# Optimization experiments

Hardware: AMD Instinct MI355X
Metric: run time of the kernel (lower is better)

The kernel has to match this reference:

```python
import jax, jax.numpy as jnp
import numpy as np

DIM = 64
N_NODES = 20000
N_EDGES = 60000
N_TORS = 1024
ACT = 6


def setup_inputs() -> dict:
    key = jax.random.key(0)
    ks = iter(jax.random.split(key, 40))
    def rn(*s):
        return jax.random.normal(next(ks), s, dtype=jnp.float32) * 0.05
    d = DIM
    inp = {}
    inp["x"] = jax.random.normal(next(ks), (N_NODES, 3), dtype=jnp.float32)
    inp["edge_attr"] = jax.random.uniform(next(ks), (N_EDGES, 7), dtype=jnp.float32)
    inp["W0"] = rn(d, 3); inp["b0"] = rn(d)
    inp["We1"] = rn(128, 7); inp["be1"] = rn(128)
    inp["We2"] = rn(d * d, 128); inp["be2"] = rn(d * d)
    inp["root"] = rn(d, d); inp["conv_b"] = rn(d)
    inp["gru_wih"] = rn(3 * d, d); inp["gru_whh"] = rn(3 * d, d)
    inp["gru_bih"] = rn(3 * d); inp["gru_bhh"] = rn(3 * d)
    inp["s2s_wi"] = rn(4 * d, 2 * d); inp["s2s_wh"] = rn(4 * d, d)
    inp["s2s_bi"] = rn(4 * d); inp["s2s_bh"] = rn(4 * d)
    inp["mem_wi"] = rn(24 * d, 6 * d); inp["mem_wh"] = rn(24 * d, 6 * d)
    inp["mem_bi"] = rn(24 * d); inp["mem_bh"] = rn(24 * d)
    inp["W1"] = rn(2 * d, 6 * d); inp["b1"] = rn(2 * d)
    inp["W2"] = rn(ACT, 2 * d); inp["b2"] = rn(ACT)
    inp["edge_index"] = jax.random.randint(next(ks), (2, N_EDGES), 0, N_NODES)
    inp["nonring"] = jax.random.randint(next(ks), (N_TORS, 4), 0, N_NODES)
    return inp


def reference(x, edge_attr, W0, b0, We1, be1, We2, be2, root, conv_b,
              gru_wih, gru_whh, gru_bih, gru_bhh,
              s2s_wi, s2s_wh, s2s_bi, s2s_bh,
              mem_wi, mem_wh, mem_bi, mem_bh,
              W1, b1, W2, b2, edge_index, nonring):
    d = DIM
    n = x.shape[0]
    src, dst = edge_index[0], edge_index[1]
    # lin0 + relu
    out = jax.nn.relu(x @ W0.T + b0)                       # [N, d]
    h = out                                                # GRU hidden
    # per-edge dim x dim weights from the edge MLP (edge_attr is loop-invariant)
    We = jax.nn.relu(edge_attr @ We1.T + be1) @ We2.T + be2
    We = We.reshape(-1, d, d)                              # [E, d, d]
    deg = jnp.zeros((n,), jnp.float32).at[dst].add(1.0)
    inv_deg = 1.0 / jnp.maximum(deg, 1.0)
    for _ in range(6):
        # NNConv: gather -> per-edge matmul -> scatter-mean, plus root transform
        msg = jnp.einsum('ed,edf->ef', out[src], We)       # [E, d]
        agg = jnp.zeros((n, d), msg.dtype).at[dst].add(msg) * inv_deg[:, None]
        m = jax.nn.relu(agg + out @ root + conv_b)
        # GRU cell (torch gate order r, z, n)
        gx = m @ gru_wih.T + gru_bih
        gh = h @ gru_whh.T + gru_bhh
        r = jax.nn.sigmoid(gx[:, :d] + gh[:, :d])
        z = jax.nn.sigmoid(gx[:, d:2 * d] + gh[:, d:2 * d])
        nn_ = jnp.tanh(gx[:, 2 * d:] + r * gh[:, 2 * d:])
        h = (1.0 - z) * nn_ + z * h
        out = h
    # Set2Set pooling, single graph (data.batch is all zeros)
    q_star = jnp.zeros((1, 2 * d), out.dtype)
    hs = jnp.zeros((1, d), out.dtype)
    cs = jnp.zeros((1, d), out.dtype)
    for _ in range(6):
        g = q_star @ s2s_wi.T + s2s_bi + hs @ s2s_wh.T + s2s_bh
        i = jax.nn.sigmoid(g[:, :d])
        f = jax.nn.sigmoid(g[:, d:2 * d])
        gg = jnp.tanh(g[:, 2 * d:3 * d])
        o = jax.nn.sigmoid(g[:, 3 * d:])
        cs = f * cs + i * gg
        hs = o * jnp.tanh(cs)
        q = hs                                             # [1, d]
        e = out @ q[0]                                     # [N]
        a = jax.nn.softmax(e)
        rvec = (a[:, None] * out).sum(0, keepdims=True)    # [1, d]
        q_star = jnp.concatenate([q, rvec], axis=1)
    pool = q_star                                          # [1, 2d]
    # faithful quirky index/view/permute + repeat_interleave concat
    t = nonring.shape[0]
    sel = out[nonring.reshape(-1)]                         # [4T, d]
    sel = sel.reshape(4 * d, t).T                          # [T, 4d]
    rep = jnp.repeat(pool.reshape(-1), t).reshape(t, 2 * d)
    z_in = jnp.concatenate([sel, rep], axis=1)             # [T, 6d]
    # memory LSTM, seq_len = 1, zero initial state (states not passed in orig)
    D6 = 6 * d
    g = z_in @ mem_wi.T + mem_bi + mem_bh                  # h0 = 0 so Wh term vanishes
    i = jax.nn.sigmoid(g[:, :D6])
    f = jax.nn.sigmoid(g[:, D6:2 * D6])
    gg = jnp.tanh(g[:, 2 * D6:3 * D6])
    o = jax.nn.sigmoid(g[:, 3 * D6:])
    cm = i * gg
    hm = o * jnp.tanh(cm)                                  # [T, 6d]
    y = jax.nn.relu(hm @ W1.T + b1) @ W2.T + b2            # [T, ACT]
    return y[None]                                         # [1, T, ACT]
```

## Files before the change

kernel.cpp:

```cpp
#include <hip/hip_runtime.h>
#include <hip/hip_bf16.h>

#define NN 20000
#define NE 60000
#define NT 1024

typedef unsigned short ushortT;
typedef __attribute__((ext_vector_type(8))) short bf16x8;
typedef __attribute__((ext_vector_type(8))) unsigned short u16x8;
typedef __attribute__((ext_vector_type(4))) float f32x4;

__device__ __forceinline__ float sigm(float x){ return 1.0f/(1.0f+expf(-x)); }
__device__ __forceinline__ float bfu2f(ushortT u){ return __uint_as_float(((unsigned)u)<<16); }
__device__ __forceinline__ ushortT f2bfu(float f){
  __hip_bfloat16 b = __float2bfloat16(f);
  return *reinterpret_cast<ushortT*>(&b);
}

__global__ void k_lin0(const float* __restrict__ x, const float* __restrict__ W0,
                       const float* __restrict__ b0, float* __restrict__ out,
                       float* __restrict__ h, ushortT* __restrict__ outbf){
  int idx = blockIdx.x*256 + threadIdx.x;
  int n = idx >> 6, j = idx & 63;
  float a = b0[j] + x[n*3+0]*W0[j*3+0] + x[n*3+1]*W0[j*3+1] + x[n*3+2]*W0[j*3+2];
  a = fmaxf(a, 0.0f);
  out[idx] = a; h[idx] = a; outbf[idx] = f2bfu(a);
}

__global__ void k_deg(const int* __restrict__ dst, float* __restrict__ deg){
  int e = blockIdx.x*256 + threadIdx.x;
  if (e < NE) atomicAdd(&deg[dst[e]], 1.0f);
}

__global__ void k_edgemlp(const float* __restrict__ ea, const float* __restrict__ We1,
                          const float* __restrict__ be1, ushortT* __restrict__ Rbf){
  int idx = blockIdx.x*256 + threadIdx.x;
  int e = idx >> 7, k = idx & 127;
  float a = be1[k];
  #pragma unroll
  for (int j = 0; j < 7; ++j) a += ea[e*7+j]*We1[k*7+j];
  Rbf[idx] = f2bfu(fmaxf(a, 0.0f));
}

#define PREP_T ((4096*128) + (1536*384) + (128*384) + 2*(192*64))
__global__ void k_prep(const float* __restrict__ We2, const float* __restrict__ memwi,
                       const float* __restrict__ W1, const float* __restrict__ gwih,
                       const float* __restrict__ gwhh,
                       ushortT* __restrict__ We2bf, ushortT* __restrict__ wmem,
                       ushortT* __restrict__ w1bf, float* __restrict__ gwih_t,
                       float* __restrict__ gwhh_t){
  int idx = blockIdx.x*256 + threadIdx.x;
  if (idx < 4096*128){ We2bf[idx] = f2bfu(We2[idx]); return; }
  idx -= 4096*128;
  if (idx < 1536*384){ wmem[idx] = f2bfu(memwi[idx]); return; }
  idx -= 1536*384;
  if (idx < 128*384){ w1bf[idx] = f2bfu(W1[idx]); return; }
  idx -= 128*384;
  if (idx < 192*64){ int r = idx / 64, c = idx % 64; gwih_t[c*192 + r] = gwih[idx]; return; }
  idx -= 192*64;
  if (idx < 192*64){ int r = idx / 64, c = idx % 64; gwhh_t[c*192 + r] = gwhh[idx]; return; }
}

#define EB 256
__global__ __launch_bounds__(256, 2) void k_fmsg(
    const ushortT* __restrict__ Rbf, const ushortT* __restrict__ We2bf,
    const float* __restrict__ be2, const ushortT* __restrict__ outbf,
    const int* __restrict__ src, const int* __restrict__ dst,
    float* __restrict__ agg)
{
  __shared__ ushortT o_sT[64][264];
  __shared__ ushortT bufB[4][4096];
  __shared__ float   be2q[64][32];
  __shared__ int     dst_s[EB];

  int tid = threadIdx.x;
  int e0 = blockIdx.x * EB;
  int fh = blockIdx.y;
  int w = tid >> 6, lane = tid & 63;
  int l15 = lane & 15, g = lane >> 4;

  auto stage = [&](int d, int b){
    #pragma unroll
    for (int i = 0; i < 2; ++i){
      int s = (w*2 + i)*64 + lane;
      int row = s >> 4, kslot = s & 15;
      const ushortT* gp = We2bf + (size_t)((d<<6) + (fh<<5) + row)*128 + ((kslot ^ (row & 7))<<3);
      __builtin_amdgcn_global_load_lds(
          (const __attribute__((address_space(1))) void*)gp,
          (__attribute__((address_space(3))) void*)&bufB[b][(size_t)s*8], 16, 0, 0);
    }
  };
  stage(0, 0); stage(1, 1); stage(2, 2);

  {
    int ge = e0 + tid;
    int sn = src[ge];
    dst_s[tid] = (ge < NE) ? dst[ge] : -1;
    const ushortT* op = outbf + (size_t)sn*64;
    #pragma unroll
    for (int i = 0; i < 8; ++i){
      u16x8 v = *reinterpret_cast<const u16x8*>(op + i*8);
      #pragma unroll
      for (int j = 0; j < 8; ++j) o_sT[i*8+j][tid] = v[j];
    }
  }
  #pragma unroll
  for (int i = 0; i < 8; ++i){
    int idx = tid*8 + i;
    int dd = idx >> 5, cc = idx & 31;
    be2q[dd][cc] = be2[(dd<<6) + (fh<<5) + cc];
  }

  bf16x8 af[4][4];
  #pragma unroll
  for (int t = 0; t < 4; ++t){
    #pragma unroll
    for (int ks = 0; ks < 4; ++ks){
      int ge = e0 + w*64 + t*16 + l15;
      bf16x8 z = {0,0,0,0,0,0,0,0};
      af[t][ks] = (ge < NE) ? *reinterpret_cast<const bf16x8*>(Rbf + (size_t)ge*128 + ks*32 + g*8) : z;
    }
  }

  f32x4 msg[4][2];
  #pragma unroll
  for (int t = 0; t < 4; ++t){
    #pragma unroll
    for (int q = 0; q < 2; ++q){ msg[t][q][0]=0.f; msg[t][q][1]=0.f; msg[t][q][2]=0.f; msg[t][q][3]=0.f; }
  }
  __syncthreads();

  auto compute = [&](int d, int b){
    bf16x8 bf0[4], bf1[4];
    #pragma unroll
    for (int ks = 0; ks < 4; ++ks){
      bf0[ks] = *reinterpret_cast<const bf16x8*>(&bufB[b][ (l15)*128    + ((((ks<<2)+g) ^ (l15&7))<<3) ]);
      bf1[ks] = *reinterpret_cast<const bf16x8*>(&bufB[b][ (16+l15)*128 + ((((ks<<2)+g) ^ (l15&7))<<3) ]);
    }
    f32x4 ac[4][2];
    #pragma unroll
    for (int t = 0; t < 4; ++t){
      #pragma unroll
      for (int q = 0; q < 2; ++q){ ac[t][q][0]=0.f; ac[t][q][1]=0.f; ac[t][q][2]=0.f; ac[t][q][3]=0.f; }
    }
    __builtin_amdgcn_s_setprio(1);
    #pragma unroll
    for (int ks = 0; ks < 4; ++ks){
      #pragma unroll
      for (int t = 0; t < 4; ++t){
        ac[t][0] = __builtin_amdgcn_mfma_f32_16x16x32_bf16(af[t][ks], bf0[ks], ac[t][0], 0, 0, 0);
        ac[t][1] = __builtin_amdgcn_mfma_f32_16x16x32_bf16(af[t][ks], bf1[ks], ac[t][1], 0, 0, 0);
      }
    }
    __builtin_amdgcn_s_setprio(0);
    float be2v0 = be2q[d][l15];
    float be2v1 = be2q[d][16 + l15];
    #pragma unroll
    for (int t = 0; t < 4; ++t){
      ushort4 ou = *reinterpret_cast<const ushort4*>(&o_sT[d][w*64 + t*16 + g*4]);
      float o0 = bfu2f(ou.x), o1 = bfu2f(ou.y), o2 = bfu2f(ou.z), o3 = bfu2f(ou.w);
      msg[t][0][0] += o0*(ac[t][0][0] + be2v0);
      msg[t][0][1] += o1*(ac[t][0][1] + be2v0);
      msg[t][0][2] += o2*(ac[t][0][2] + be2v0);
      msg[t][0][3] += o3*(ac[t][0][3] + be2v0);
      msg[t][1][0] += o0*(ac[t][1][0] + be2v1);
      msg[t][1][1] += o1*(ac[t][1][1] + be2v1);
      msg[t][1][2] += o2*(ac[t][1][2] + be2v1);
      msg[t][1][3] += o3*(ac[t][1][3] + be2v1);
    }
  };

  for (int d = 0; d < 61; ++d){
    asm volatile("s_waitcnt vmcnt(4)" ::: "memory");
    __builtin_amdgcn_sched_barrier(0);
    __builtin_amdgcn_s_barrier();
    __builtin_amdgcn_sched_barrier(0);
    stage(d + 3, (d + 3) & 3);
    compute(d, d & 3);
  }
  asm volatile("s_waitcnt vmcnt(4)" ::: "memory");
  __builtin_amdgcn_sched_barrier(0);
  __builtin_amdgcn_s_barrier();
  __builtin_amdgcn_sched_barrier(0);
  compute(61, 61 & 3);
  asm volatile("s_waitcnt vmcnt(2)" ::: "memory");
  __builtin_amdgcn_sched_barrier(0);
  __builtin_amdgcn_s_barrier();
  __builtin_amdgcn_sched_barrier(0);
  compute(62, 62 & 3);
  asm volatile("s_waitcnt vmcnt(0)" ::: "memory");
  __builtin_amdgcn_sched_barrier(0);
  __builtin_amdgcn_s_barrier();
  __builtin_amdgcn_sched_barrier(0);
  compute(63, 63 & 3);

  #pragma unroll
  for (int t = 0; t < 4; ++t){
    #pragma unroll
    for (int r = 0; r < 4; ++r){
      int el = w*64 + t*16 + g*4 + r;
      int tn = dst_s[el];
      if (tn >= 0){
        atomicAdd(&agg[(size_t)tn*64 + (fh<<5) + l15],      msg[t][0][r]);
        atomicAdd(&agg[(size_t)tn*64 + (fh<<5) + 16 + l15], msg[t][1][r]);
      }
    }
  }
}

__global__ void k_gru(const float* __restrict__ agg_in, const float* __restrict__ deg,
                      const float* __restrict__ root, const float* __restrict__ conv_b,
                      const float* __restrict__ wih_t, const float* __restrict__ whh_t,
                      const float* __restrict__ bih, const float* __restrict__ bhh,
                      float* __restrict__ out, float* __restrict__ h,
                      ushortT* __restrict__ outbf){
  __shared__ float os[16][64], hsm[16][64], ms[16][64];
  float* agg = const_cast<float*>(agg_in);
  int tid = threadIdx.x;
  int j = tid & 63, sub = tid >> 6;
  int n0 = blockIdx.x * 16;
  #pragma unroll
  for (int i = 0; i < 4; ++i){
    int nl = sub + 4*i;
    os[nl][j]  = out[(size_t)(n0+nl)*64 + j];
    hsm[nl][j] = h[(size_t)(n0+nl)*64 + j];
  }
  __syncthreads();
  float a[4];
  #pragma unroll
  for (int i = 0; i < 4; ++i){
    int nl = sub + 4*i;
    float inv = 1.0f/fmaxf(deg[n0+nl], 1.0f);
    a[i] = agg[(size_t)(n0+nl)*64 + j]*inv + conv_b[j];
    agg[(size_t)(n0+nl)*64 + j] = 0.0f;
  }
  for (int d = 0; d < 64; ++d){
    float rdj = root[d*64 + j];
    #pragma unroll
    for (int i = 0; i < 4; ++i) a[i] += os[sub + 4*i][d]*rdj;
  }
  #pragma unroll
  for (int i = 0; i < 4; ++i) ms[sub + 4*i][j] = fmaxf(a[i], 0.0f);
  __syncthreads();
  float gxr[4], gxz[4], gxn[4], ghr[4], ghz[4], ghn[4];
  #pragma unroll
  for (int i = 0; i < 4; ++i){
    gxr[i] = bih[j];     gxz[i] = bih[64+j];  gxn[i] = bih[128+j];
    ghr[i] = bhh[j];     ghz[i] = bhh[64+j];  ghn[i] = bhh[128+j];
  }
  for (int d = 0; d < 64; ++d){
    float wir = wih_t[d*192 + j], wiz = wih_t[d*192 + 64 + j], win = wih_t[d*192 + 128 + j];
    float whr = whh_t[d*192 + j], whz = whh_t[d*192 + 64 + j], whn = whh_t[d*192 + 128 + j];
    #pragma unroll
    for (int i = 0; i < 4; ++i){
      float mv = ms[sub + 4*i][d], hv = hsm[sub + 4*i][d];
      gxr[i] += mv*wir; gxz[i] += mv*wiz; gxn[i] += mv*win;
      ghr[i] += hv*whr; ghz[i] += hv*whz; ghn[i] += hv*whn;
    }
  }
  #pragma unroll
  for (int i = 0; i < 4; ++i){
    int nl = sub + 4*i;
    float r = sigm(gxr[i]+ghr[i]), zg = sigm(gxz[i]+ghz[i]);
    float nn_ = tanhf(gxn[i] + r*ghn[i]);
    float hn = (1.0f - zg)*nn_ + zg*hsm[nl][j];
    h[(size_t)(n0+nl)*64 + j]   = hn;
    out[(size_t)(n0+nl)*64 + j] = hn;
    outbf[(size_t)(n0+nl)*64 + j] = f2bfu(hn);
  }
}

__global__ void k_s2s2(const float* __restrict__ out, const float* __restrict__ wi,
                       const float* __restrict__ wh, const float* __restrict__ bi,
                       const float* __restrict__ bh, float* __restrict__ st, int it){
  const float* sr = st + it*256;
  float* sw = st + (it+1)*256;
  __shared__ float qs[128], hsl[64], gg[256];
  __shared__ float ob[128*65], wl[128], zred[128], part[256];
  int tid = threadIdx.x;
  int n0 = blockIdx.x * 128;

  if (tid < 64) qs[tid] = sr[tid];
  else if (tid < 128){
    float Z = sr[192];
    qs[tid] = (Z != 0.0f) ? sr[128 + (tid-64)]/Z : 0.0f;
  }
  __syncthreads();
  {
    float a = bi[tid] + bh[tid];
    #pragma unroll 8
    for (int k = 0; k < 128; ++k) a += qs[k]*wi[tid*128 + k];
    #pragma unroll 8
    for (int k = 0; k < 64;  ++k) a += sr[k]*wh[tid*64 + k];
    gg[tid] = a;
  }
  __syncthreads();
  if (tid < 64){
    float iv = sigm(gg[tid]), fv = sigm(gg[64+tid]);
    float gv = tanhf(gg[128+tid]), ov = sigm(gg[192+tid]);
    float c = fv*sr[64+tid] + iv*gv;
    float hnew = ov*tanhf(c);
    hsl[tid] = hnew;
    if (blockIdx.x == 0){ sw[64+tid] = c; sw[tid] = hnew; }
  }
  #pragma unroll
  for (int rr = 0; rr < 8; ++rr){
    int idx = rr*1024 + tid*4;
    int nl = idx >> 6, jj = idx & 63;
    float4 v = make_float4(0.f,0.f,0.f,0.f);
    if (n0 + nl < NN) v = *reinterpret_cast<const float4*>(&out[(size_t)(n0+nl)*64 + jj]);
    ob[nl*65 + jj + 0] = v.x; ob[nl*65 + jj + 1] = v.y;
    ob[nl*65 + jj + 2] = v.z; ob[nl*65 + jj + 3] = v.w;
  }
  __syncthreads();
  if (tid < 128){
    float e = 0.f;
    #pragma unroll 8
    for (int jj = 0; jj < 64; ++jj) e += ob[tid*65 + jj]*hsl[jj];
    float wv = (n0 + tid < NN) ? expf(e) : 0.f;
    wl[tid] = wv; zred[tid] = wv;
  }
  __syncthreads();
  if (tid < 64) zred[tid] += zred[tid + 64];
  __syncthreads();
  if (tid < 32) zred[tid] += zred[tid + 32];
  __syncthreads();
  if (tid < 16) zred[tid] += zred[tid + 16];
  __syncthreads();
  if (tid < 8) zred[tid] += zred[tid + 8];
  __syncthreads();
  if (tid == 0){
    float z = zred[0]+zred[1]+zred[2]+zred[3]+zred[4]+zred[5]+zred[6]+zred[7];
    atomicAdd(&sw[192], z);
  }
  {
    int gq = tid >> 6, d = tid & 63;
    float acc = 0.f;
    #pragma unroll 8
    for (int i = 0; i < 32; ++i){
      int nl = gq*32 + i;
      acc += wl[nl]*ob[nl*65 + d];
    }
    part[tid] = acc;
  }
  __syncthreads();
  if (tid < 64)
    atomicAdd(&sw[128 + tid], part[tid] + part[64+tid] + part[128+tid] + part[192+tid]);
}

__global__ void k_z(const float* __restrict__ out, const float* __restrict__ st,
                    const int* __restrict__ nonring, ushortT* __restrict__ zbf){
  const float* s6 = st + 6*256;
  int idx = blockIdx.x*256 + threadIdx.x;
  int t = idx / 384, c = idx % 384;
  float v;
  if (c < 256){
    int a = c*16 + (t >> 6);
    int node = nonring[a];
    v = out[(size_t)node*64 + (t & 63)];
  } else {
    int pi = t >> 3;
    v = (pi < 64) ? s6[pi] : s6[128 + (pi - 64)] / s6[192];
  }
  zbf[idx] = f2bfu(v);
}

__global__ __launch_bounds__(256) void k_mem2(
    const ushortT* __restrict__ zbf, const ushortT* __restrict__ wmem,
    const float* __restrict__ membi, const float* __restrict__ membh,
    ushortT* __restrict__ hmbf){
  int tid = threadIdx.x;
  int w = tid >> 6, lane = tid & 63;
  int l15 = lane & 15, g = lane >> 4;
  int m0 = blockIdx.x * 32;
  int jw = blockIdx.y * 64 + w * 16;

  f32x4 ai[2], ag[2], ao[2];
  #pragma unroll
  for (int m = 0; m < 2; ++m){
    #pragma unroll
    for (int r = 0; r < 4; ++r){ ai[m][r]=0.f; ag[m][r]=0.f; ao[m][r]=0.f; }
  }
  const ushortT* a0p = zbf + (size_t)(m0 + l15)*384 + g*8;
  const ushortT* a1p = zbf + (size_t)(m0 + 16 + l15)*384 + g*8;
  const ushortT* bip = wmem + (size_t)(jw + l15)*384 + g*8;
  const ushortT* bgp = wmem + (size_t)(768 + jw + l15)*384 + g*8;
  const ushortT* bop = wmem + (size_t)(1152 + jw + l15)*384 + g*8;
  #pragma unroll
  for (int ks = 0; ks < 12; ++ks){
    bf16x8 a0 = *reinterpret_cast<const bf16x8*>(a0p + ks*32);
    bf16x8 a1 = *reinterpret_cast<const bf16x8*>(a1p + ks*32);
    bf16x8 bi = *reinterpret_cast<const bf16x8*>(bip + ks*32);
    bf16x8 bg = *reinterpret_cast<const bf16x8*>(bgp + ks*32);
    bf16x8 bo = *reinterpret_cast<const bf16x8*>(bop + ks*32);
    ai[0] = __builtin_amdgcn_mfma_f32_16x16x32_bf16(a0, bi, ai[0], 0, 0, 0);
    ai[1] = __builtin_amdgcn_mfma_f32_16x16x32_bf16(a1, bi, ai[1], 0, 0, 0);
    ag[0] = __builtin_amdgcn_mfma_f32_16x16x32_bf16(a0, bg, ag[0], 0, 0, 0);
    ag[1] = __builtin_amdgcn_mfma_f32_16x16x32_bf16(a1, bg, ag[1], 0, 0, 0);
    ao[0] = __builtin_amdgcn_mfma_f32_16x16x32_bf16(a0, bo, ao[0], 0, 0, 0);
    ao[1] = __builtin_amdgcn_mfma_f32_16x16x32_bf16(a1, bo, ao[1], 0, 0, 0);
  }
  int j = jw + l15;
  float bI = membi[j]        + membh[j];
  float bG = membi[768 + j]  + membh[768 + j];
  float bO = membi[1152 + j] + membh[1152 + j];
  #pragma unroll
  for (int m = 0; m < 2; ++m){
    #pragma unroll
    for (int r = 0; r < 4; ++r){
      int t = m0 + m*16 + g*4 + r;
      float gi = ai[m][r] + bI;
      float gG = ag[m][r] + bG;
      float go = ao[m][r] + bO;
      float cm = sigm(gi)*tanhf(gG);
      hmbf[(size_t)t*384 + j] = f2bfu(sigm(go)*tanhf(cm));
    }
  }
}

__global__ __launch_bounds__(256) void k_fin1(
    const ushortT* __restrict__ hmbf, const ushortT* __restrict__ w1bf,
    const float* __restrict__ b1, float* __restrict__ hid){
  int tid = threadIdx.x;
  int w = tid >> 6, lane = tid & 63;
  int l15 = lane & 15, g = lane >> 4;
  int m0 = blockIdx.x * 32;
  int cw = blockIdx.y * 64 + w * 16;

  f32x4 acc[2];
  #pragma unroll
  for (int m = 0; m < 2; ++m){
    #pragma unroll
    for (int r = 0; r < 4; ++r) acc[m][r] = 0.f;
  }
  const ushortT* a0p = hmbf + (size_t)(m0 + l15)*384 + g*8;
  const ushortT* a1p = hmbf + (size_t)(m0 + 16 + l15)*384 + g*8;
  const ushortT* bp  = w1bf + (size_t)(cw + l15)*384 + g*8;
  #pragma unroll
  for (int ks = 0; ks < 12; ++ks){
    bf16x8 a0 = *reinterpret_cast<const bf16x8*>(a0p + ks*32);
    bf16x8 a1 = *reinterpret_cast<const bf16x8*>(a1p + ks*32);
    bf16x8 b  = *reinterpret_cast<const bf16x8*>(bp + ks*32);
    acc[0] = __builtin_amdgcn_mfma_f32_16x16x32_bf16(a0, b, acc[0], 0, 0, 0);
    acc[1] = __builtin_amdgcn_mfma_f32_16x16x32_bf16(a1, b, acc[1], 0, 0, 0);
  }
  int c = cw + l15;
  float bv = b1[c];
  #pragma unroll
  for (int m = 0; m < 2; ++m){
    #pragma unroll
    for (int r = 0; r < 4; ++r){
      int t = m0 + m*16 + g*4 + r;
      hid[(size_t)t*128 + c] = fmaxf(acc[m][r] + bv, 0.0f);
    }
  }
}

__global__ void k_fin2(const float* __restrict__ hid, const float* __restrict__ W2,
                       const float* __restrict__ b2, float* __restrict__ y){
  int tid = threadIdx.x;
  int t = blockIdx.x*32 + (tid >> 3);
  int j = tid & 7;
  if (j >= 6) return;
  float a = b2[j];
  const float* hp = hid + (size_t)t*128;
  const float* wp = W2 + j*128;
  #pragma unroll 8
  for (int k = 0; k < 128; ++k) a += hp[k]*wp[k];
  y[t*6 + j] = a;
}

extern "C" void kernel_launch(void* const* d_in, const int* in_sizes, int n_in,
                              void* d_out, int out_size, void* d_ws, size_t ws_size,
                              hipStream_t stream){
  const float* x      = (const float*)d_in[0];
  const float* ea     = (const float*)d_in[1];
  const float* W0     = (const float*)d_in[2];
  const float* b0     = (const float*)d_in[3];
  const float* We1    = (const float*)d_in[4];
  const float* be1    = (const float*)d_in[5];
  const float* We2    = (const float*)d_in[6];
  const float* be2    = (const float*)d_in[7];
  const float* root   = (const float*)d_in[8];
  const float* conv_b = (const float*)d_in[9];
  const float* gwih   = (const float*)d_in[10];
  const float* gwhh   = (const float*)d_in[11];
  const float* gbih   = (const float*)d_in[12];
  const float* gbhh   = (const float*)d_in[13];
  const float* s2swi  = (const float*)d_in[14];
  const float* s2swh  = (const float*)d_in[15];
  const float* s2sbi  = (const float*)d_in[16];
  const float* s2sbh  = (const float*)d_in[17];
  const float* memwi  = (const float*)d_in[18];
  const float* membi  = (const float*)d_in[20];
  const float* membh  = (const float*)d_in[21];
  const float* W1     = (const float*)d_in[22];
  const float* b1     = (const float*)d_in[23];
  const float* W2     = (const float*)d_in[24];
  const float* b2     = (const float*)d_in[25];
  const int*   eidx   = (const int*)d_in[26];
  const int*   nonr   = (const int*)d_in[27];
  const int* src = eidx, *dst = eidx + NE;
  float* y = (float*)d_out;

  char* wsb = (char*)d_ws;
  size_t off = 0;
  auto alloc = [&](size_t bytes){ size_t o = off; off += (bytes + 255) & ~(size_t)255; return o; };
  float* out    = (float*)(wsb + alloc((size_t)NN*64*4));
  float* h      = (float*)(wsb + alloc((size_t)NN*64*4));
  float* agg    = (float*)(wsb + alloc((size_t)NN*64*4));
  float* deg    = (float*)(wsb + alloc((size_t)NN*4));
  float* st     = (float*)(wsb + alloc(7*256*4));
  float* hid    = (float*)(wsb + alloc((size_t)NT*128*4));
  float* gwih_t = (float*)(wsb + alloc((size_t)192*64*4));
  float* gwhh_t = (float*)(wsb + alloc((size_t)192*64*4));
  ushortT* Rbf  = (ushortT*)(wsb + alloc((size_t)NE*128*2));
  ushortT* We2bf= (ushortT*)(wsb + alloc((size_t)4096*128*2));
  ushortT* wmem = (ushortT*)(wsb + alloc((size_t)1536*384*2));
  ushortT* w1bf = (ushortT*)(wsb + alloc((size_t)128*384*2));
  ushortT* zbf  = (ushortT*)(wsb + alloc((size_t)NT*384*2));
  ushortT* hmbf = (ushortT*)(wsb + alloc((size_t)NT*384*2));
  ushortT* outbf= (ushortT*)(wsb + alloc((size_t)NN*64*2));
  (void)ws_size; (void)n_in; (void)in_sizes; (void)out_size;

  hipMemsetAsync(deg, 0, (size_t)NN*4, stream);
  hipMemsetAsync(st, 0, 7*256*4, stream);
  hipMemsetAsync(agg, 0, (size_t)NN*64*4, stream);
  k_lin0<<<NN*64/256, 256, 0, stream>>>(x, W0, b0, out, h, outbf);
  k_deg<<<(NE+255)/256, 256, 0, stream>>>(dst, deg);
  k_edgemlp<<<NE*128/256, 256, 0, stream>>>(ea, We1, be1, Rbf);
  k_prep<<<(PREP_T+255)/256, 256, 0, stream>>>(We2, memwi, W1, gwih, gwhh,
                                               We2bf, wmem, w1bf, gwih_t, gwhh_t);

  for (int it = 0; it < 6; ++it){
    k_fmsg<<<dim3((NE + EB - 1)/EB, 2), 256, 0, stream>>>(Rbf, We2bf, be2, outbf, src, dst, agg);
    k_gru<<<NN/16, 256, 0, stream>>>(agg, deg, root, conv_b, gwih_t, gwhh_t,
                                     gbih, gbhh, out, h, outbf);
  }

  for (int it = 0; it < 6; ++it){
    k_s2s2<<<(NN + 127)/128, 256, 0, stream>>>(out, s2swi, s2swh, s2sbi, s2sbh, st, it);
  }

  k_z<<<NT*384/256, 256, 0, stream>>>(out, st, nonr, zbf);
  k_mem2<<<dim3(32, 6), 256, 0, stream>>>(zbf, wmem, membi, membh, hmbf);
  k_fin1<<<dim3(32, 2), 256, 0, stream>>>(hmbf, w1bf, b1, hid);
  k_fin2<<<32, 256, 0, stream>>>(hid, W2, b2, y);
}
```

Baseline: 764.3 us.

## Software-pipeline LDS fragment reads one stage ahead of MFMA compute

Splits the per-slice compute into a fragment-read phase and an MFMA phase. The B fragments and o values for slice d+1 are read from LDS while the MFMAs for slice d run, so LDS latency is hidden behind matrix work. To keep slice d+1 ready one iteration early, the global-load wait is tightened from vmcnt(4) to vmcnt(2). This doubles the fragment registers held per thread, which may lower occupancy, and it shortens the prefetch distance for global loads.

After: 783.6 us. 1.03x slower.

```diff
diff --git a/kernel.cpp b/kernel.cpp
--- a/kernel.cpp
+++ b/kernel.cpp
@@ -130,13 +130,21 @@
   }
   __syncthreads();
 
-  auto compute = [&](int d, int b){
-    bf16x8 bf0[4], bf1[4];
+  bf16x8 bcur0[4], bcur1[4], bnxt0[4], bnxt1[4];
+  ushort4 ocur[4], onxt[4];
+
+  auto readfrags = [&](int d, int b, bf16x8* f0, bf16x8* f1, ushort4* ov){
     #pragma unroll
     for (int ks = 0; ks < 4; ++ks){
-      bf0[ks] = *reinterpret_cast<const bf16x8*>(&bufB[b][ (l15)*128    + ((((ks<<2)+g) ^ (l15&7))<<3) ]);
-      bf1[ks] = *reinterpret_cast<const bf16x8*>(&bufB[b][ (16+l15)*128 + ((((ks<<2)+g) ^ (l15&7))<<3) ]);
-    }
+      f0[ks] = *reinterpret_cast<const bf16x8*>(&bufB[b][ (l15)*128    + ((((ks<<2)+g) ^ (l15&7))<<3) ]);
+      f1[ks] = *reinterpret_cast<const bf16x8*>(&bufB[b][ (16+l15)*128 + ((((ks<<2)+g) ^ (l15&7))<<3) ]);
+    }
+    #pragma unroll
+    for (int t = 0; t < 4; ++t)
+      ov[t] = *reinterpret_cast<const ushort4*>(&o_sT[d][w*64 + t*16 + g*4]);
+  };
+
+  auto domfma = [&](int d, const bf16x8* f0, const bf16x8* f1, const ushort4* ov){
     f32x4 ac[4][2];
     #pragma unroll
     for (int t = 0; t < 4; ++t){
@@ -148,8 +156,8 @@
     for (int ks = 0; ks < 4; ++ks){
       #pragma unroll
       for (int t = 0; t < 4; ++t){
-        ac[t][0] = __builtin_amdgcn_mfma_f32_16x16x32_bf16(af[t][ks], bf0[ks], ac[t][0], 0, 0, 0);
-        ac[t][1] = __builtin_amdgcn_mfma_f32_16x16x32_bf16(af[t][ks], bf1[ks], ac[t][1], 0, 0, 0);
+        ac[t][0] = __builtin_amdgcn_mfma_f32_16x16x32_bf16(af[t][ks], f0[ks], ac[t][0], 0, 0, 0);
+        ac[t][1] = __builtin_amdgcn_mfma_f32_16x16x32_bf16(af[t][ks], f1[ks], ac[t][1], 0, 0, 0);
       }
     }
     __builtin_amdgcn_s_setprio(0);
@@ -157,8 +165,7 @@
     float be2v1 = be2q[d][16 + l15];
     #pragma unroll
     for (int t = 0; t < 4; ++t){
-      ushort4 ou = *reinterpret_cast<const ushort4*>(&o_sT[d][w*64 + t*16 + g*4]);
-      float o0 = bfu2f(ou.x), o1 = bfu2f(ou.y), o2 = bfu2f(ou.z), o3 = bfu2f(ou.w);
+      float o0 = bfu2f(ov[t].x), o1 = bfu2f(ov[t].y), o2 = bfu2f(ov[t].z), o3 = bfu2f(ov[t].w);
       msg[t][0][0] += o0*(ac[t][0][0] + be2v0);
       msg[t][0][1] += o1*(ac[t][0][1] + be2v0);
       msg[t][0][2] += o2*(ac[t][0][2] + be2v0);
@@ -170,29 +177,38 @@
     }
   };
 
+  readfrags(0, 0, bcur0, bcur1, ocur);
+
   for (int d = 0; d < 61; ++d){
-    asm volatile("s_waitcnt vmcnt(4)" ::: "memory");
+    asm volatile("s_waitcnt vmcnt(2)" ::: "memory");
     __builtin_amdgcn_sched_barrier(0);
     __builtin_amdgcn_s_barrier();
     __builtin_amdgcn_sched_barrier(0);
     stage(d + 3, (d + 3) & 3);
-    compute(d, d & 3);
-  }
-  asm volatile("s_waitcnt vmcnt(4)" ::: "memory");
-  __builtin_amdgcn_sched_barrier(0);
-  __builtin_amdgcn_s_barrier();
-  __builtin_amdgcn_sched_barrier(0);
-  compute(61, 61 & 3);
+    readfrags(d + 1, (d + 1) & 3, bnxt0, bnxt1, onxt);
+    domfma(d, bcur0, bcur1, ocur);
+    #pragma unroll
+    for (int ks = 0; ks < 4; ++ks){ bcur0[ks] = bnxt0[ks]; bcur1[ks] = bnxt1[ks]; }
+    #pragma unroll
+    for (int t = 0; t < 4; ++t) ocur[t] = onxt[t];
+  }
   asm volatile("s_waitcnt vmcnt(2)" ::: "memory");
   __builtin_amdgcn_sched_barrier(0);
   __builtin_amdgcn_s_barrier();
   __builtin_amdgcn_sched_barrier(0);
-  compute(62, 62 & 3);
+  readfrags(62, 62 & 3, bnxt0, bnxt1, onxt);
+  domfma(61, bcur0, bcur1, ocur);
+  #pragma unroll
+  for (int ks = 0; ks < 4; ++ks){ bcur0[ks] = bnxt0[ks]; bcur1[ks] = bnxt1[ks]; }
+  #pragma unroll
+  for (int t = 0; t < 4; ++t) ocur[t] = onxt[t];
   asm volatile("s_waitcnt vmcnt(0)" ::: "memory");
   __builtin_amdgcn_sched_barrier(0);
   __builtin_amdgcn_s_barrier();
   __builtin_amdgcn_sched_barrier(0);
-  compute(63, 63 & 3);
+  readfrags(63, 63 & 3, bnxt0, bnxt1, onxt);
+  domfma(62, bcur0, bcur1, ocur);
+  domfma(63, bnxt0, bnxt1, onxt);
 
   #pragma unroll
   for (int t = 0; t < 4; ++t){
```

## Rewrite GRU node update with bf16 MFMA for root and gate matmuls

Applied to the files above, without the earlier changes.

Replaces the scalar fp32 GRU/root-transform kernel with an MFMA-based version that computes the root transform and the input/hidden gate matmuls as bf16 16x16x32 tiles over 32 nodes per block. Weights are pre-converted to bf16 (root transposed) in the prep kernel, and a bf16 copy of the hidden state is kept. The intent is to remove the heavy per-thread FMA loops and LDS reads of the old kernel. The cost is bf16 rounding of the hidden state and messages inside the recurrence, which may reduce accuracy.

Measured after the change: 680.1 us. 11.0% less time.

```diff
diff --git a/kernel.cpp b/kernel.cpp
--- a/kernel.cpp
+++ b/kernel.cpp
@@ -19,12 +19,15 @@
 
 __global__ void k_lin0(const float* __restrict__ x, const float* __restrict__ W0,
                        const float* __restrict__ b0, float* __restrict__ out,
-                       float* __restrict__ h, ushortT* __restrict__ outbf){
+                       float* __restrict__ h, ushortT* __restrict__ outbf,
+                       ushortT* __restrict__ hbf){
   int idx = blockIdx.x*256 + threadIdx.x;
   int n = idx >> 6, j = idx & 63;
   float a = b0[j] + x[n*3+0]*W0[j*3+0] + x[n*3+1]*W0[j*3+1] + x[n*3+2]*W0[j*3+2];
   a = fmaxf(a, 0.0f);
-  out[idx] = a; h[idx] = a; outbf[idx] = f2bfu(a);
+  out[idx] = a; h[idx] = a;
+  ushortT u = f2bfu(a);
+  outbf[idx] = u; hbf[idx] = u;
 }
 
 __global__ void k_deg(const int* __restrict__ dst, float* __restrict__ deg){
@@ -42,13 +45,13 @@
   Rbf[idx] = f2bfu(fmaxf(a, 0.0f));
 }
 
-#define PREP_T ((4096*128) + (1536*384) + (128*384) + 2*(192*64))
+#define PREP_T ((4096*128) + (1536*384) + (128*384) + (192*64) + (192*64) + (64*64))
 __global__ void k_prep(const float* __restrict__ We2, const float* __restrict__ memwi,
                        const float* __restrict__ W1, const float* __restrict__ gwih,
-                       const float* __restrict__ gwhh,
+                       const float* __restrict__ gwhh, const float* __restrict__ root,
                        ushortT* __restrict__ We2bf, ushortT* __restrict__ wmem,
-                       ushortT* __restrict__ w1bf, float* __restrict__ gwih_t,
-                       float* __restrict__ gwhh_t){
+                       ushortT* __restrict__ w1bf, ushortT* __restrict__ gwihbf,
+                       ushortT* __restrict__ gwhhbf, ushortT* __restrict__ rootTbf){
   int idx = blockIdx.x*256 + threadIdx.x;
   if (idx < 4096*128){ We2bf[idx] = f2bfu(We2[idx]); return; }
   idx -= 4096*128;
@@ -56,9 +59,11 @@
   idx -= 1536*384;
   if (idx < 128*384){ w1bf[idx] = f2bfu(W1[idx]); return; }
   idx -= 128*384;
-  if (idx < 192*64){ int r = idx / 64, c = idx % 64; gwih_t[c*192 + r] = gwih[idx]; return; }
+  if (idx < 192*64){ gwihbf[idx] = f2bfu(gwih[idx]); return; }
   idx -= 192*64;
-  if (idx < 192*64){ int r = idx / 64, c = idx % 64; gwhh_t[c*192 + r] = gwhh[idx]; return; }
+  if (idx < 192*64){ gwhhbf[idx] = f2bfu(gwhh[idx]); return; }
+  idx -= 192*64;
+  if (idx < 64*64){ int d = idx >> 6, j = idx & 63; rootTbf[j*64 + d] = f2bfu(root[idx]); }
 }
 
 #define EB 256
@@ -208,65 +213,103 @@
   }
 }
 
-__global__ void k_gru(const float* __restrict__ agg_in, const float* __restrict__ deg,
-                      const float* __restrict__ root, const float* __restrict__ conv_b,
-                      const float* __restrict__ wih_t, const float* __restrict__ whh_t,
-                      const float* __restrict__ bih, const float* __restrict__ bhh,
-                      float* __restrict__ out, float* __restrict__ h,
-                      ushortT* __restrict__ outbf){
-  __shared__ float os[16][64], hsm[16][64], ms[16][64];
+__global__ __launch_bounds__(256) void k_gru2(
+    const float* __restrict__ agg_in, const float* __restrict__ deg,
+    const ushortT* __restrict__ rootT, const float* __restrict__ conv_b,
+    const ushortT* __restrict__ wih, const ushortT* __restrict__ whh,
+    const float* __restrict__ bih, const float* __restrict__ bhh,
+    float* __restrict__ out, float* __restrict__ h,
+    ushortT* __restrict__ outbf, ushortT* __restrict__ hbf)
+{
+  __shared__ ushortT mbf[32*64];
   float* agg = const_cast<float*>(agg_in);
   int tid = threadIdx.x;
-  int j = tid & 63, sub = tid >> 6;
-  int n0 = blockIdx.x * 16;
-  #pragma unroll
-  for (int i = 0; i < 4; ++i){
-    int nl = sub + 4*i;
-    os[nl][j]  = out[(size_t)(n0+nl)*64 + j];
-    hsm[nl][j] = h[(size_t)(n0+nl)*64 + j];
-  }
-  __syncthreads();
-  float a[4];
-  #pragma unroll
-  for (int i = 0; i < 4; ++i){
-    int nl = sub + 4*i;
-    float inv = 1.0f/fmaxf(deg[n0+nl], 1.0f);
-    a[i] = agg[(size_t)(n0+nl)*64 + j]*inv + conv_b[j];
-    agg[(size_t)(n0+nl)*64 + j] = 0.0f;
-  }
-  for (int d = 0; d < 64; ++d){
-    float rdj = root[d*64 + j];
-    #pragma unroll
-    for (int i = 0; i < 4; ++i) a[i] += os[sub + 4*i][d]*rdj;
-  }
-  #pragma unroll
-  for (int i = 0; i < 4; ++i) ms[sub + 4*i][j] = fmaxf(a[i], 0.0f);
-  __syncthreads();
-  float gxr[4], gxz[4], gxn[4], ghr[4], ghz[4], ghn[4];
-  #pragma unroll
-  for (int i = 0; i < 4; ++i){
-    gxr[i] = bih[j];     gxz[i] = bih[64+j];  gxn[i] = bih[128+j];
-    ghr[i] = bhh[j];     ghz[i] = bhh[64+j];  ghn[i] = bhh[128+j];
-  }
-  for (int d = 0; d < 64; ++d){
-    float wir = wih_t[d*192 + j], wiz = wih_t[d*192 + 64 + j], win = wih_t[d*192 + 128 + j];
-    float whr = whh_t[d*192 + j], whz = whh_t[d*192 + 64 + j], whn = whh_t[d*192 + 128 + j];
-    #pragma unroll
-    for (int i = 0; i < 4; ++i){
-      float mv = ms[sub + 4*i][d], hv = hsm[sub + 4*i][d];
-      gxr[i] += mv*wir; gxz[i] += mv*wiz; gxn[i] += mv*win;
-      ghr[i] += hv*whr; ghz[i] += hv*whz; ghn[i] += hv*whn;
-    }
-  }
-  #pragma unroll
-  for (int i = 0; i < 4; ++i){
-    int nl = sub + 4*i;
-    float r = sigm(gxr[i]+ghr[i]), zg = sigm(gxz[i]+ghz[i]);
-    float nn_ = tanhf(gxn[i] + r*ghn[i]);
-    float hn = (1.0f - zg)*nn_ + zg*hsm[nl][j];
-    h[(size_t)(n0+nl)*64 + j]   = hn;
-    out[(size_t)(n0+nl)*64 + j] = hn;
-    outbf[(size_t)(n0+nl)*64 + j] = f2bfu(hn);
+  int w = tid >> 6, lane = tid & 63;
+  int l15 = lane & 15, g = lane >> 4;
+  int n0 = blockIdx.x * 32;
+  int j = w*16 + l15;
+
+  f32x4 acc1[2];
+  #pragma unroll
+  for (int rt = 0; rt < 2; ++rt){ acc1[rt][0]=0.f; acc1[rt][1]=0.f; acc1[rt][2]=0.f; acc1[rt][3]=0.f; }
+  bf16x8 ah[2][2];
+  #pragma unroll
+  for (int ks = 0; ks < 2; ++ks){
+    bf16x8 b = *reinterpret_cast<const bf16x8*>(rootT + (size_t)j*64 + g*8 + ks*32);
+    #pragma unroll
+    for (int rt = 0; rt < 2; ++rt){
+      bf16x8 a = *reinterpret_cast<const bf16x8*>(outbf + (size_t)(n0 + rt*16 + l15)*64 + g*8 + ks*32);
+      acc1[rt] = __builtin_amdgcn_mfma_f32_16x16x32_bf16(a, b, acc1[rt], 0, 0, 0);
+      ah[rt][ks] = *reinterpret_cast<const bf16x8*>(hbf + (size_t)(n0 + rt*16 + l15)*64 + g*8 + ks*32);
+    }
+  }
+  {
+    float cb = conv_b[j];
+    #pragma unroll
+    for (int rt = 0; rt < 2; ++rt){
+      #pragma unroll
+      for (int r = 0; r < 4; ++r){
+        int row = rt*16 + g*4 + r;
+        int node = n0 + row;
+        float inv = 1.0f/fmaxf(deg[node], 1.0f);
+        float mval = fmaxf(acc1[rt][r] + agg[(size_t)node*64 + j]*inv + cb, 0.0f);
+        agg[(size_t)node*64 + j] = 0.0f;
+        int gran = (j >> 3) ^ (row & 7);
+        mbf[row*64 + (gran<<3) + (j & 7)] = f2bfu(mval);
+      }
+    }
+  }
+  __syncthreads();
+
+  f32x4 gx[3][2], gh[3][2];
+  #pragma unroll
+  for (int ci = 0; ci < 3; ++ci){
+    #pragma unroll
+    for (int rt = 0; rt < 2; ++rt){
+      gx[ci][rt][0]=0.f; gx[ci][rt][1]=0.f; gx[ci][rt][2]=0.f; gx[ci][rt][3]=0.f;
+      gh[ci][rt][0]=0.f; gh[ci][rt][1]=0.f; gh[ci][rt][2]=0.f; gh[ci][rt][3]=0.f;
+    }
+  }
+  #pragma unroll
+  for (int ks = 0; ks < 2; ++ks){
+    bf16x8 am[2];
+    #pragma unroll
+    for (int rt = 0; rt < 2; ++rt){
+      int arow = rt*16 + l15;
+      int agran = (g + ks*4) ^ (l15 & 7);
+      am[rt] = *reinterpret_cast<const bf16x8*>(&mbf[arow*64 + (agran<<3)]);
+    }
+    #pragma unroll
+    for (int ci = 0; ci < 3; ++ci){
+      int c = (w + ci*4)*16 + l15;
+      bf16x8 bx = *reinterpret_cast<const bf16x8*>(wih + (size_t)c*64 + g*8 + ks*32);
+      bf16x8 bh = *reinterpret_cast<const bf16x8*>(whh + (size_t)c*64 + g*8 + ks*32);
+      #pragma unroll
+      for (int rt = 0; rt < 2; ++rt){
+        gx[ci][rt] = __builtin_amdgcn_mfma_f32_16x16x32_bf16(am[rt], bx, gx[ci][rt], 0, 0, 0);
+        gh[ci][rt] = __builtin_amdgcn_mfma_f32_16x16x32_bf16(ah[rt][ks], bh, gh[ci][rt], 0, 0, 0);
+      }
+    }
+  }
+  float bxr = bih[j], bxz = bih[64+j], bxn = bih[128+j];
+  float bhr = bhh[j], bhz = bhh[64+j], bhn = bhh[128+j];
+  #pragma unroll
+  for (int rt = 0; rt < 2; ++rt){
+    #pragma unroll
+    for (int r = 0; r < 4; ++r){
+      int node = n0 + rt*16 + g*4 + r;
+      float gxr = gx[0][rt][r] + bxr, gxz = gx[1][rt][r] + bxz, gxn = gx[2][rt][r] + bxn;
+      float ghr = gh[0][rt][r] + bhr, ghz = gh[1][rt][r] + bhz, ghn = gh[2][rt][r] + bhn;
+      float rr = sigm(gxr + ghr), zz = sigm(gxz + ghz);
+      float nn_ = tanhf(gxn + rr*ghn);
+      float hold = h[(size_t)node*64 + j];
+      float hn = (1.0f - zz)*nn_ + zz*hold;
+      h[(size_t)node*64 + j]   = hn;
+      out[(size_t)node*64 + j] = hn;
+      ushortT u = f2bfu(hn);
+      outbf[(size_t)node*64 + j] = u;
+      hbf[(size_t)node*64 + j]   = u;
+    }
   }
 }
 
@@ -512,8 +555,6 @@
   float* deg    = (float*)(wsb + alloc((size_t)NN*4));
   float* st     = (float*)(wsb + alloc(7*256*4));
   float* hid    = (float*)(wsb + alloc((size_t)NT*128*4));
-  float* gwih_t = (float*)(wsb + alloc((size_t)192*64*4));
-  float* gwhh_t = (float*)(wsb + alloc((size_t)192*64*4));
   ushortT* Rbf  = (ushortT*)(wsb + alloc((size_t)NE*128*2));
   ushortT* We2bf= (ushortT*)(wsb + alloc((size_t)4096*128*2));
   ushortT* wmem = (ushortT*)(wsb + alloc((size_t)1536*384*2));
@@ -521,21 +562,25 @@
   ushortT* zbf  = (ushortT*)(wsb + alloc((size_t)NT*384*2));
   ushortT* hmbf = (ushortT*)(wsb + alloc((size_t)NT*384*2));
   ushortT* outbf= (ushortT*)(wsb + alloc((size_t)NN*64*2));
+  ushortT* hbf  = (ushortT*)(wsb + alloc((size_t)NN*64*2));
+  ushortT* gwihbf = (ushortT*)(wsb + alloc((size_t)192*64*2));
+  ushortT* gwhhbf = (ushortT*)(wsb + alloc((size_t)192*64*2));
+  ushortT* rootTbf= (ushortT*)(wsb + alloc((size_t)64*64*2));
   (void)ws_size; (void)n_in; (void)in_sizes; (void)out_size;
 
   hipMemsetAsync(deg, 0, (size_t)NN*4, stream);
   hipMemsetAsync(st, 0, 7*256*4, stream);
   hipMemsetAsync(agg, 0, (size_t)NN*64*4, stream);
-  k_lin0<<<NN*64/256, 256, 0, stream>>>(x, W0, b0, out, h, outbf);
+  k_lin0<<<NN*64/256, 256, 0, stream>>>(x, W0, b0, out, h, outbf, hbf);
   k_deg<<<(NE+255)/256, 256, 0, stream>>>(dst, deg);
   k_edgemlp<<<NE*128/256, 256, 0, stream>>>(ea, We1, be1, Rbf);
-  k_prep<<<(PREP_T+255)/256, 256, 0, stream>>>(We2, memwi, W1, gwih, gwhh,
-                                               We2bf, wmem, w1bf, gwih_t, gwhh_t);
+  k_prep<<<(PREP_T+255)/256, 256, 0, stream>>>(We2, memwi, W1, gwih, gwhh, root,
+                                               We2bf, wmem, w1bf, gwihbf, gwhhbf, rootTbf);
 
   for (int it = 0; it < 6; ++it){
     k_fmsg<<<dim3((NE + EB - 1)/EB, 2), 256, 0, stream>>>(Rbf, We2bf, be2, outbf, src, dst, agg);
-    k_gru<<<NN/16, 256, 0, stream>>>(agg, deg, root, conv_b, gwih_t, gwhh_t,
-                                     gbih, gbhh, out, h, outbf);
+    k_gru2<<<NN/32, 256, 0, stream>>>(agg, deg, rootTbf, conv_b, gwihbf, gwhhbf,
+                                      gbih, gbhh, out, h, outbf, hbf);
   }
 
   for (int it = 0; it < 6; ++it){
```
